# Optimization experiments

Hardware: AMD Instinct MI355X
Metric: run time of the kernel (lower is better)

The kernel has to match this reference:

```python
import jax, jax.numpy as jnp
import numpy as np
import math

DIM = 128      # head_dim (multiple of 2)
BASE = 10000
B, H, L = 2, 16, 8192


def setup_inputs() -> dict:
    key = jax.random.key(0)
    # Resonance RoPE buffers: snap each wavelength to the nearest integer.
    inv_freq = 1.0 / BASE ** (np.arange(0, DIM, 2, dtype=np.float32) / DIM)
    r_wavelengths = np.round(2.0 * math.pi / inv_freq).astype(np.float32)   # [DIM//2]
    r_inv_freq = (2.0 * math.pi / r_wavelengths).astype(np.float32)         # [DIM//2]
    x = jax.random.normal(key, (B, H, L, DIM), dtype=jnp.float32)
    position_ids = jnp.tile(jnp.arange(L, dtype=jnp.int32)[None, :], (B, 1))  # [B, L]
    return {
        "x": x,
        "position_ids": position_ids,
        "r_inv_freq": jnp.asarray(r_inv_freq),
        "r_wavelengths": jnp.asarray(r_wavelengths),
    }


def reference(x, position_ids, r_inv_freq, r_wavelengths):
    # seq_len as in torch: max position id + 1 (traced scalar)
    seq_len = jnp.max(position_ids) + 1
    Lq = position_ids.shape[1]
    D2 = r_inv_freq.shape[0]

    w = r_wavelengths.astype(jnp.int32)            # [D2] integer wavelengths
    l = jnp.arange(Lq, dtype=jnp.int32)            # [Lq]
    # Per-frequency wraparound index: tile-of-first-w positions == gather at l % w
    # when seq_len >= wavelength; otherwise plain positions (identity index).
    idx = jnp.where(w[:, None] <= seq_len, l[None, :] % w[:, None], l[None, :])  # [D2, Lq]

    gathered = position_ids[:, idx].astype(jnp.float32)        # [B, D2, Lq]
    freqs = jnp.transpose(gathered, (0, 2, 1)) * r_inv_freq    # [B, Lq, D2]

    emb = jnp.concatenate([freqs, freqs], axis=-1)             # [B, Lq, DIM]
    cos = jnp.cos(emb).astype(x.dtype)
    sin = jnp.sin(emb).astype(x.dtype)
    return cos, sin
```

## Files before the change

### kernel.cpp

```cpp
#include <hip/hip_runtime.h>
#include <math.h>

#define BB   2
#define LL   8192
#define DIMM 128
#define D2   64

__global__ void seqlen_kernel(const int* __restrict__ pos, int n, int* __restrict__ out) {
    int t = threadIdx.x;
    int m = -2147483647 - 1;
    for (int i = t; i < n; i += 256) m = max(m, pos[i]);
    #pragma unroll
    for (int off = 32; off > 0; off >>= 1)
        m = max(m, __shfl_down(m, off, 64));
    __shared__ int smem[4];
    if ((t & 63) == 0) smem[t >> 6] = m;
    __syncthreads();
    if (t == 0) {
        int r = max(max(smem[0], smem[1]), max(smem[2], smem[3]));
        out[0] = r + 1;
    }
}

__global__ void rope_kernel(const int* __restrict__ pos_ids,
                            const float* __restrict__ inv_freq,
                            const float* __restrict__ wavelengths,
                            const int* __restrict__ seq_len_p,
                            float* __restrict__ out) {
    int tid = blockIdx.x * blockDim.x + threadIdx.x;
    int d = tid & (D2 - 1);
    int l = (tid >> 6) & (LL - 1);
    int b = tid >> 19;

    int seq_len = seq_len_p[0];
    int w = (int)wavelengths[d];
    float fi = inv_freq[d];

    int widx = (w <= seq_len) ? (l % w) : l;
    float p = (float)pos_ids[b * LL + widx];
    float ang = p * fi;
    float s = __sinf(ang);
    float c = __cosf(ang);

    float* cosb = out;
    float* sinb = out + (size_t)BB * LL * DIMM;
    size_t base = (size_t)b * LL * DIMM + (size_t)l * DIMM + d;
    cosb[base]      = c;
    cosb[base + D2] = c;
    sinb[base]      = s;
    sinb[base + D2] = s;
}

extern "C" void kernel_launch(void* const* d_in, const int* in_sizes, int n_in,
                              void* d_out, int out_size, void* d_ws, size_t ws_size,
                              hipStream_t stream) {
    const int*   pos  = (const int*)d_in[1];
    const float* finv = (const float*)d_in[2];
    const float* wav  = (const float*)d_in[3];
    float* out = (float*)d_out;
    int*   ws  = (int*)d_ws;

    int n_pos = in_sizes[1];
    seqlen_kernel<<<1, 256, 0, stream>>>(pos, n_pos, ws);

    int total = BB * LL * D2;
    rope_kernel<<<total / 256, 256, 0, stream>>>(pos, finv, wav, ws, out);
}
```

Measured before the change: 183.4 us.

## Fuse seq_len reduction into RoPE kernel with persistent waves and float2 stores

Merges the separate max-reduction kernel into the RoPE kernel: each of 256 blocks redundantly computes seq_len from position_ids with int4 loads, which removes one launch and the dependency through workspace memory. Each wave then walks a contiguous set of rows, with each lane producing two adjacent frequencies and writing them as float2 stores. The trade-off is that every block re-reads the 64 KB position array and there are fewer threads in flight to hide store latency.

```diff
diff --git a/kernel.cpp b/kernel.cpp
--- a/kernel.cpp
+++ b/kernel.cpp
@@ -6,49 +6,76 @@
 #define DIMM 128
 #define D2   64
 
-__global__ void seqlen_kernel(const int* __restrict__ pos, int n, int* __restrict__ out) {
-    int t = threadIdx.x;
+#define NBLOCKS 256
+#define NTHREADS 256
+
+__global__ void __launch_bounds__(NTHREADS)
+rope_fused_kernel(const int* __restrict__ pos_ids, int n_pos,
+                  const float* __restrict__ inv_freq,
+                  const float* __restrict__ wavelengths,
+                  float* __restrict__ out) {
+    const int t = threadIdx.x;
+
     int m = -2147483647 - 1;
-    for (int i = t; i < n; i += 256) m = max(m, pos[i]);
+    const int n4 = n_pos >> 2;
+    const int4* p4 = (const int4*)pos_ids;
+    for (int i = t; i < n4; i += NTHREADS) {
+        int4 v = p4[i];
+        m = max(max(m, v.x), max(max(v.y, v.z), v.w));
+    }
+    for (int i = (n4 << 2) + t; i < n_pos; i += NTHREADS) m = max(m, pos_ids[i]);
     #pragma unroll
     for (int off = 32; off > 0; off >>= 1)
         m = max(m, __shfl_down(m, off, 64));
-    __shared__ int smem[4];
+    __shared__ int smem[NTHREADS / 64];
+    __shared__ int s_seqlen;
     if ((t & 63) == 0) smem[t >> 6] = m;
     __syncthreads();
     if (t == 0) {
-        int r = max(max(smem[0], smem[1]), max(smem[2], smem[3]));
-        out[0] = r + 1;
+        int r = smem[0];
+        #pragma unroll
+        for (int i = 1; i < NTHREADS / 64; i++) r = max(r, smem[i]);
+        s_seqlen = r + 1;
     }
-}
+    __syncthreads();
+    const int seq_len = s_seqlen;
 
-__global__ void rope_kernel(const int* __restrict__ pos_ids,
-                            const float* __restrict__ inv_freq,
-                            const float* __restrict__ wavelengths,
-                            const int* __restrict__ seq_len_p,
-                            float* __restrict__ out) {
-    int tid = blockIdx.x * blockDim.x + threadIdx.x;
-    int d = tid & (D2 - 1);
-    int l = (tid >> 6) & (LL - 1);
-    int b = tid >> 19;
+    const int lane = t & 63;
+    const int wv   = t >> 6;
+    const int d0 = (2 * lane) & (D2 - 1);
+    const int d1 = d0 + 1;
+    const int w0 = (int)wavelengths[d0];
+    const int w1 = (int)wavelengths[d1];
+    const float f0 = inv_freq[d0];
+    const float f1 = inv_freq[d1];
+    const bool mod0 = (w0 <= seq_len);
+    const bool mod1 = (w1 <= seq_len);
 
-    int seq_len = seq_len_p[0];
-    int w = (int)wavelengths[d];
-    float fi = inv_freq[d];
+    const int gw = blockIdx.x * (NTHREADS / 64) + wv;
+    const int NWAVES = NBLOCKS * (NTHREADS / 64);
+    const int ROWS = BB * LL;
+    const int rpw = ROWS / NWAVES;
 
-    int widx = (w <= seq_len) ? (l % w) : l;
-    float p = (float)pos_ids[b * LL + widx];
-    float ang = p * fi;
-    float s = __sinf(ang);
-    float c = __cosf(ang);
+    float2* cosb = (float2*)out;
+    float2* sinb = (float2*)(out + (size_t)BB * LL * DIMM);
 
-    float* cosb = out;
-    float* sinb = out + (size_t)BB * LL * DIMM;
-    size_t base = (size_t)b * LL * DIMM + (size_t)l * DIMM + d;
-    cosb[base]      = c;
-    cosb[base + D2] = c;
-    sinb[base]      = s;
-    sinb[base + D2] = s;
+    #pragma unroll 4
+    for (int k = 0; k < rpw; k++) {
+        const int r = gw * rpw + k;
+        const int b = r >> 13;
+        const int l = r & (LL - 1);
+
+        const int i0 = mod0 ? (l % w0) : l;
+        const int i1 = mod1 ? (l % w1) : l;
+        const float p0 = (float)pos_ids[b * LL + i0];
+        const float p1 = (float)pos_ids[b * LL + i1];
+        const float a0 = p0 * f0;
+        const float a1 = p1 * f1;
+
+        const size_t rowbase = ((size_t)r * DIMM >> 1) + lane;
+        cosb[rowbase] = make_float2(__cosf(a0), __cosf(a1));
+        sinb[rowbase] = make_float2(__sinf(a0), __sinf(a1));
+    }
 }
 
 extern "C" void kernel_launch(void* const* d_in, const int* in_sizes, int n_in,
@@ -58,11 +85,6 @@
     const float* finv = (const float*)d_in[2];
     const float* wav  = (const float*)d_in[3];
     float* out = (float*)d_out;
-    int*   ws  = (int*)d_ws;
 
-    int n_pos = in_sizes[1];
-    seqlen_kernel<<<1, 256, 0, stream>>>(pos, n_pos, ws);
-
-    int total = BB * LL * D2;
-    rope_kernel<<<total / 256, 256, 0, stream>>>(pos, finv, wav, ws, out);
+    rope_fused_kernel<<<NBLOCKS, NTHREADS, 0, stream>>>(pos, in_sizes[1], finv, wav, out);
 }
```

Result: faster. 173.0 us (-5.7%).
